# Kernel optimization log

Hardware: AMD Instinct MI355X
Metric: run time of the kernel (lower is better)

## Reference

```python
import jax, jax.numpy as jnp
import numpy as np

B, S, H = 1, 2048, 1024
NH, NKV, HD = 16, 4, 64
I, E, K = 2816, 8, 2
WIN = 512
EPS = 1e-5


def setup_inputs() -> dict:
    key = jax.random.key(0)
    ks = jax.random.split(key, 8)
    sd = 0.02
    return {
        "hidden_states": jax.random.normal(ks[0], (B, S, H), jnp.float32),
        "positions": jnp.arange(S, dtype=jnp.int64),
        "w_qkv": jax.random.normal(ks[1], ((NH + 2 * NKV) * HD, H), jnp.float32) * sd,
        "w_o": jax.random.normal(ks[2], (H, NH * HD), jnp.float32) * sd,
        "router_w": jax.random.normal(ks[3], (E, H), jnp.float32) * sd,
        "ws": jax.random.normal(ks[4], (E, 2 * I, H), jnp.float32) * sd,
        "w2s": jax.random.normal(ks[5], (E, H, I), jnp.float32) * sd,
        "ln1_w": jnp.ones((H,), jnp.float32),
        "ln2_w": jnp.ones((H,), jnp.float32),
    }


def _rmsnorm(x, w):
    return x * jax.lax.rsqrt(jnp.mean(x * x, axis=-1, keepdims=True) + EPS) * w


def reference(hidden_states, positions, w_qkv, w_o, router_w, ws, w2s, ln1_w, ln2_w):
    # residual is None on entry -> residual = input, then input_layernorm
    residual = hidden_states
    x = _rmsnorm(hidden_states, ln1_w)

    # qkv projection (torch Linear: y = x @ W.T), GQA split
    qkv = jnp.einsum("bsh,oh->bso", x, w_qkv)
    q_size, kv_size = NH * HD, NKV * HD
    q = qkv[..., :q_size].reshape(B, S, NH, HD)
    k = qkv[..., q_size:q_size + kv_size].reshape(B, S, NKV, HD)
    v = qkv[..., q_size + kv_size:].reshape(B, S, NKV, HD)
    rep = NH // NKV
    k = jnp.repeat(k, rep, axis=2)  # [B,S,NH,HD]
    v = jnp.repeat(v, rep, axis=2)

    scale = HD ** -0.5
    scores = jnp.einsum("bqhd,bkhd->bhqk", q, k) * scale
    i = jnp.arange(S)[:, None]
    j = jnp.arange(S)[None, :]
    mask = (j <= i) & ((i - j) < WIN)  # causal sliding window
    scores = jnp.where(mask, scores, jnp.finfo(scores.dtype).min)
    attn = jax.nn.softmax(scores, axis=-1)
    o = jnp.einsum("bhqk,bkhd->bqhd", attn, v).reshape(B, S, NH * HD)
    attn_out = jnp.einsum("bso,ho->bsh", o, w_o)

    # pre_moe_layernorm with residual: x += residual; residual = x; x = norm(x)
    x2 = attn_out + residual
    residual2 = x2
    h = _rmsnorm(x2, ln2_w)

    # MoE: router softmax, top-k (renormalize=False), per-expert SwiGLU FFN
    t = h.reshape(-1, H)  # [T,H]
    logits = jnp.einsum("th,eh->te", t, router_w)
    probs = jax.nn.softmax(logits, axis=-1)
    vals, idx = jax.lax.top_k(probs, K)  # [T,K]
    w_dense = jnp.sum(vals[:, :, None] * jax.nn.one_hot(idx, E, dtype=t.dtype), axis=1)  # [T,E]

    out = jnp.zeros_like(t)
    for e in range(E):
        gu = jnp.einsum("th,ih->ti", t, ws[e])  # [T,2I]
        g, u = gu[:, :I], gu[:, I:]
        a = jax.nn.silu(g) * u
        y = jnp.einsum("ti,hi->th", a, w2s[e])
        out = out + w_dense[:, e:e + 1] * y

    return out.reshape(B, S, H), residual2
```

## Files before the change

kernel.cpp:

```cpp
#include <hip/hip_runtime.h>
#include <stdint.h>

typedef unsigned short u16;
typedef __attribute__((ext_vector_type(8))) short short8;
typedef __attribute__((ext_vector_type(4))) float f32x4;

constexpr int SEQ   = 2048;
constexpr int HID   = 1024;
constexpr int NHEAD = 16;
constexpr int QKVD  = 1536;
constexpr int FFI   = 2816;
constexpr int NEXP  = 8;
constexpr int WINSZ = 512;
#define EPSF 1e-5f

__device__ __forceinline__ u16 f2bf(float f) {
  union { unsigned int i; float f; } v; v.f = f;
  unsigned int i = v.i;
  return (u16)((i + 0x7fffu + ((i >> 16) & 1u)) >> 16);
}

__device__ __forceinline__ void gload_lds16(const void* g, void* l) {
  __builtin_amdgcn_global_load_lds((__attribute__((address_space(1))) void*)g,
                                   (__attribute__((address_space(3))) void*)l,
                                   16, 0, 0);
}

#define MFMA_BF16(a, b, c) __builtin_amdgcn_mfma_f32_16x16x32_bf16(a, b, c, 0, 0, 0)

constexpr int CN1 = QKVD * HID / 4;
constexpr int CN2 = HID * HID / 4;
constexpr int CN3 = NEXP * 2 * FFI * HID / 4;
constexpr int CN4 = NEXP * HID * FFI / 4;
constexpr int CN_SMALL = CN1 + CN2;
constexpr int CN_BIG   = CN3 + CN4;
constexpr int NCONV_BLK = CN_BIG / 1024;
constexpr int NATTN_BLK = (SEQ / 64) * NHEAD;

__global__ __launch_bounds__(256) void k_prep(
    const float* __restrict__ x, const float* __restrict__ w, u16* __restrict__ y,
    const float* __restrict__ wqkv, const float* __restrict__ wo,
    u16* __restrict__ dq, u16* __restrict__ dwo) {
  const int bid = blockIdx.x, tid = threadIdx.x;
  __shared__ float red[4];
  if (bid < SEQ) {
    const int wid = tid >> 6, lane = tid & 63;
    const float* xr = x + (size_t)bid * HID;
    float4 v = *(const float4*)&xr[tid * 4];
    float ss = v.x * v.x + v.y * v.y + v.z * v.z + v.w * v.w;
#pragma unroll
    for (int m = 1; m < 64; m <<= 1) ss += __shfl_xor(ss, m);
    if (lane == 0) red[wid] = ss;
    __syncthreads();
    ss = red[0] + red[1] + red[2] + red[3];
    float sc = rsqrtf(ss * (1.0f / HID) + EPSF);
    float4 wv = *(const float4*)&w[tid * 4];
    ushort4 o;
    o.x = f2bf(v.x * sc * wv.x);
    o.y = f2bf(v.y * sc * wv.y);
    o.z = f2bf(v.z * sc * wv.z);
    o.w = f2bf(v.w * sc * wv.w);
    *(ushort4*)&y[(size_t)bid * HID + tid * 4] = o;
    return;
  }
  int j = (bid - SEQ) * 1024 + tid;
#pragma unroll
  for (int t = 0; t < 4; ++t) {
    int i = j + t * 256;
    const float* s; u16* d;
    if (i < CN1) { s = wqkv; d = dq; } else { i -= CN1; s = wo; d = dwo; }
    float4 v = ((const float4*)s)[i];
    ushort4 o;
    o.x = f2bf(v.x); o.y = f2bf(v.y); o.z = f2bf(v.z); o.w = f2bf(v.w);
    ((ushort4*)d)[i] = o;
  }
}

__global__ __launch_bounds__(256, 2) void k_gemm_bt(
    const u16* __restrict__ A, const u16* __restrict__ B,
    void* __restrict__ Cout, int N, int K, int KT, int wf32) {
  __shared__ u16 As[128 * 64];
  __shared__ u16 Bs[64 * 64];
  const int tid = threadIdx.x, wid = tid >> 6, lane = tid & 63;
  const int quad = lane >> 4, l16 = lane & 15;
  const int wr = wid >> 1, wc = wid & 1;
  const int m0 = blockIdx.y * 128, n0 = blockIdx.x * 64;
  const int M = gridDim.y * 128;
  const int kbase = blockIdx.z * KT * 64;
  const int sr = lane >> 3, sc = (lane & 7) * 8;
  f32x4 acc[4][2] = {};
  for (int kt = 0; kt < KT; ++kt) {
    const int k0 = kbase + (kt << 6);
#pragma unroll
    for (int it = 0; it < 4; ++it) {
      int seg = wid * 4 + it;
      int row = seg * 8 + sr;
      gload_lds16(&A[(size_t)(m0 + row) * K + k0 + sc], &As[seg * 512]);
    }
#pragma unroll
    for (int it = 0; it < 2; ++it) {
      int seg = wid * 2 + it;
      int row = seg * 8 + sr;
      gload_lds16(&B[(size_t)(n0 + row) * K + k0 + sc], &Bs[seg * 512]);
    }
    __syncthreads();
#pragma unroll
    for (int ks = 0; ks < 2; ++ks) {
      short8 af[4], bf[2];
#pragma unroll
      for (int t = 0; t < 4; ++t)
        af[t] = *(const short8*)&As[(64 * wr + 16 * t + l16) * 64 + ks * 32 + quad * 8];
#pragma unroll
      for (int t = 0; t < 2; ++t)
        bf[t] = *(const short8*)&Bs[(32 * wc + 16 * t + l16) * 64 + ks * 32 + quad * 8];
#pragma unroll
      for (int mt = 0; mt < 4; ++mt)
#pragma unroll
        for (int nt = 0; nt < 2; ++nt)
          acc[mt][nt] = MFMA_BF16(af[mt], bf[nt], acc[mt][nt]);
    }
    __syncthreads();
  }
  if (wf32) {
    float* C = (float*)Cout + (size_t)blockIdx.z * M * N;
#pragma unroll
    for (int mt = 0; mt < 4; ++mt)
#pragma unroll
      for (int r = 0; r < 4; ++r) {
        int row = m0 + 64 * wr + 16 * mt + quad * 4 + r;
#pragma unroll
        for (int nt = 0; nt < 2; ++nt) {
          int col = n0 + 32 * wc + 16 * nt + l16;
          C[(size_t)row * N + col] = acc[mt][nt][r];
        }
      }
  } else {
    u16* C = (u16*)Cout;
#pragma unroll
    for (int mt = 0; mt < 4; ++mt)
#pragma unroll
      for (int r = 0; r < 4; ++r) {
        int row = m0 + 64 * wr + 16 * mt + quad * 4 + r;
#pragma unroll
        for (int nt = 0; nt < 2; ++nt) {
          int col = n0 + 32 * wc + 16 * nt + l16;
          C[(size_t)row * N + col] = f2bf(acc[mt][nt][r]);
        }
      }
  }
}

__global__ __launch_bounds__(256, 2) void k_attn_conv(
    const u16* __restrict__ qkv, u16* __restrict__ o,
    const float* __restrict__ ws, const float* __restrict__ w2s,
    u16* __restrict__ dws, u16* __restrict__ dw2) {
  const int bid = blockIdx.x;
  const int tid = threadIdx.x;
  if (bid >= NATTN_BLK) {
    int j = (bid - NATTN_BLK) * 1024 + tid;
#pragma unroll
    for (int t = 0; t < 4; ++t) {
      int i = j + t * 256;
      const float* s; u16* d;
      if (i < CN3) { s = ws; d = dws; } else { i -= CN3; s = w2s; d = dw2; }
      float4 v = ((const float4*)s)[i];
      ushort4 u;
      u.x = f2bf(v.x); u.y = f2bf(v.y); u.z = f2bf(v.z); u.w = f2bf(v.w);
      ((ushort4*)d)[i] = u;
    }
    return;
  }
  const int qb = bid & 31;
  const int h  = bid >> 5;
  const int q0 = qb * 64;
  const int g = h >> 2;
  __shared__ u16 Qs[64 * 72], Ks[64 * 72], Vt[64 * 72], Ps[64 * 72];
  const int wid = tid >> 6, lane = tid & 63;
  const int quad = lane >> 4, l16 = lane & 15;

#pragma unroll
  for (int it = 0; it < 2; ++it) {
    int idx = it * 256 + tid;
    int row = idx >> 3, c8 = (idx & 7) * 8;
    *(short8*)&Qs[row * 72 + c8] =
        *(const short8*)&qkv[(size_t)(q0 + row) * QKVD + h * 64 + c8];
  }

  f32x4 oacc[4] = {};
  float mrun[4], lrun[4];
#pragma unroll
  for (int r = 0; r < 4; ++r) { mrun[r] = -1e30f; lrun[r] = 0.f; }

  const int ktlo = (q0 >= WINSZ) ? ((q0 - WINSZ + 1) >> 6) : 0;
  const int kthi = qb;
  for (int kt = ktlo; kt <= kthi; ++kt) {
#pragma unroll
    for (int it = 0; it < 2; ++it) {
      int idx = it * 256 + tid;
      int row = idx >> 3, c8 = (idx & 7) * 8;
      *(short8*)&Ks[row * 72 + c8] =
          *(const short8*)&qkv[(size_t)(kt * 64 + row) * QKVD + 1024 + g * 64 + c8];
    }
#pragma unroll
    for (int it = 0; it < 8; ++it) {
      int idx = it * 256 + tid;
      int key = idx >> 5;
      int d = (idx & 31) * 2;
      unsigned int u = *(const unsigned int*)&qkv[(size_t)(kt * 64 + key) * QKVD + 1280 + g * 64 + d];
      Vt[d * 72 + key] = (u16)(u & 0xffffu);
      Vt[(d + 1) * 72 + key] = (u16)(u >> 16);
    }
    __syncthreads();

    f32x4 sa[4] = {};
#pragma unroll
    for (int ks = 0; ks < 2; ++ks) {
      short8 af = *(const short8*)&Qs[(16 * wid + l16) * 72 + ks * 32 + quad * 8];
#pragma unroll
      for (int ct = 0; ct < 4; ++ct) {
        short8 bf = *(const short8*)&Ks[(16 * ct + l16) * 72 + ks * 32 + quad * 8];
        sa[ct] = MFMA_BF16(af, bf, sa[ct]);
      }
    }

    float pvv[4][4];
#pragma unroll
    for (int r = 0; r < 4; ++r) {
      int i = q0 + 16 * wid + quad * 4 + r;
      float mx = -1e30f;
#pragma unroll
      for (int ct = 0; ct < 4; ++ct) {
        int j = kt * 64 + 16 * ct + l16;
        float v = sa[ct][r] * 0.125f;
        bool ok = (j <= i) && (i - j < WINSZ);
        v = ok ? v : -1e30f;
        pvv[ct][r] = v;
        mx = fmaxf(mx, v);
      }
#pragma unroll
      for (int m = 1; m < 16; m <<= 1) mx = fmaxf(mx, __shfl_xor(mx, m));
      float mnew = fmaxf(mrun[r], mx);
      float alpha = __expf(mrun[r] - mnew);
      float s = 0.f;
#pragma unroll
      for (int ct = 0; ct < 4; ++ct) {
        float p = (pvv[ct][r] > -1e29f) ? __expf(pvv[ct][r] - mnew) : 0.f;
        pvv[ct][r] = p;
        s += p;
      }
#pragma unroll
      for (int m = 1; m < 16; m <<= 1) s += __shfl_xor(s, m);
      lrun[r] = lrun[r] * alpha + s;
      mrun[r] = mnew;
#pragma unroll
      for (int ct = 0; ct < 4; ++ct) oacc[ct][r] *= alpha;
    }
#pragma unroll
    for (int ct = 0; ct < 4; ++ct)
#pragma unroll
      for (int r = 0; r < 4; ++r)
        Ps[(16 * wid + quad * 4 + r) * 72 + 16 * ct + l16] = f2bf(pvv[ct][r]);
    __syncthreads();

#pragma unroll
    for (int ks = 0; ks < 2; ++ks) {
      short8 af = *(const short8*)&Ps[(16 * wid + l16) * 72 + ks * 32 + quad * 8];
#pragma unroll
      for (int ct = 0; ct < 4; ++ct) {
        short8 bf = *(const short8*)&Vt[(16 * ct + l16) * 72 + ks * 32 + quad * 8];
        oacc[ct] = MFMA_BF16(af, bf, oacc[ct]);
      }
    }
    __syncthreads();
  }

#pragma unroll
  for (int ct = 0; ct < 4; ++ct)
#pragma unroll
    for (int r = 0; r < 4; ++r) {
      int row = q0 + 16 * wid + quad * 4 + r;
      float v = oacc[ct][r] / lrun[r];
      o[(size_t)row * HID + h * 64 + 16 * ct + l16] = f2bf(v);
    }
}

__global__ __launch_bounds__(256) void k_rms2_router(
    const float* __restrict__ o0, const float* __restrict__ o1,
    const float* __restrict__ hs, const float* __restrict__ ln2,
    const float* __restrict__ rw, float* __restrict__ out1,
    u16* __restrict__ T, int* __restrict__ counts,
    int* __restrict__ tok_idx, int* __restrict__ tok_slot,
    float* __restrict__ tok_pw) {
  const int tkn = blockIdx.x, tid = threadIdx.x, wid = tid >> 6, lane = tid & 63;
  const size_t base = (size_t)tkn * HID + tid * 4;
  float4 a = *(const float4*)&o0[base];
  float4 b = *(const float4*)&o1[base];
  float4 h = *(const float4*)&hs[base];
  float4 v;
  v.x = a.x + b.x + h.x; v.y = a.y + b.y + h.y;
  v.z = a.z + b.z + h.z; v.w = a.w + b.w + h.w;
  *(float4*)&out1[base] = v;
  float ss = v.x * v.x + v.y * v.y + v.z * v.z + v.w * v.w;
#pragma unroll
  for (int m = 1; m < 64; m <<= 1) ss += __shfl_xor(ss, m);
  __shared__ float red[4];
  if (lane == 0) red[wid] = ss;
  __syncthreads();
  ss = red[0] + red[1] + red[2] + red[3];
  float sc = rsqrtf(ss * (1.0f / HID) + EPSF);
  float4 lw = *(const float4*)&ln2[tid * 4];
  float t0 = v.x * sc * lw.x;
  float t1 = v.y * sc * lw.y;
  float t2 = v.z * sc * lw.z;
  float t3 = v.w * sc * lw.w;
  ushort4 o;
  o.x = f2bf(t0); o.y = f2bf(t1); o.z = f2bf(t2); o.w = f2bf(t3);
  *(ushort4*)&T[(size_t)tkn * HID + tid * 4] = o;

  float p[8];
#pragma unroll
  for (int e = 0; e < 8; ++e) {
    float4 r = *(const float4*)&rw[e * HID + tid * 4];
    p[e] = t0 * r.x + t1 * r.y + t2 * r.z + t3 * r.w;
  }
#pragma unroll
  for (int e = 0; e < 8; ++e)
#pragma unroll
    for (int m = 1; m < 64; m <<= 1) p[e] += __shfl_xor(p[e], m);
  __shared__ float pr[4][8];
  if (lane == 0)
#pragma unroll
    for (int e = 0; e < 8; ++e) pr[wid][e] = p[e];
  __syncthreads();
  if (tid == 0) {
    float lg[8];
#pragma unroll
    for (int e = 0; e < 8; ++e) lg[e] = pr[0][e] + pr[1][e] + pr[2][e] + pr[3][e];
    float mx = lg[0];
#pragma unroll
    for (int e = 1; e < 8; ++e) mx = fmaxf(mx, lg[e]);
    float ex[8], se = 0.f;
#pragma unroll
    for (int e = 0; e < 8; ++e) { ex[e] = __expf(lg[e] - mx); se += ex[e]; }
    int b0 = 0;
#pragma unroll
    for (int e = 1; e < 8; ++e) if (lg[e] > lg[b0]) b0 = e;
    int b1 = (b0 == 0) ? 1 : 0;
#pragma unroll
    for (int e = 0; e < 8; ++e) if (e != b0 && lg[e] > lg[b1]) b1 = e;
    float inv = 1.0f / se;
    int s0 = atomicAdd(&counts[b0], 1);
    tok_idx[b0 * SEQ + s0] = tkn;
    tok_slot[2 * tkn] = b0 * SEQ + s0;
    tok_pw[2 * tkn] = ex[b0] * inv;
    int s1 = atomicAdd(&counts[b1], 1);
    tok_idx[b1 * SEQ + s1] = tkn;
    tok_slot[2 * tkn + 1] = b1 * SEQ + s1;
    tok_pw[2 * tkn + 1] = ex[b1] * inv;
  }
}

__global__ void k_offsets(const int* __restrict__ counts, int* __restrict__ offs) {
  if (threadIdx.x == 0 && blockIdx.x == 0) {
    int s = 0;
    for (int e = 0; e < NEXP; ++e) { offs[e] = s; s += counts[e]; }
    offs[NEXP] = s;
  }
}

__global__ __launch_bounds__(512, 4) void k_moe_gu(
    const u16* __restrict__ T, const u16* __restrict__ Wgu,
    const int* __restrict__ counts, const int* __restrict__ offs,
    const int* __restrict__ tok_idx, u16* __restrict__ Abuf) {
  const int e = blockIdx.z;
  const int cnt = counts[e];
  const int m0 = blockIdx.y * 256;
  if (m0 >= cnt) return;
  const int n0 = blockIdx.x * 64;
  const u16* We = Wgu + (size_t)e * 2 * FFI * HID;
  const int* ti = tok_idx + e * SEQ;
  const int aoff = offs[e];
  __shared__ u16 As[256 * 64], Bg[64 * 64], Bu[64 * 64];
  const int tid = threadIdx.x, wid = tid >> 6, lane = tid & 63;
  const int quad = lane >> 4, l16 = lane & 15;
  const int wr = wid >> 1, wc = wid & 1;
  const int sr = lane >> 3, sc = (lane & 7) * 8;
  int tokrow[4];
#pragma unroll
  for (int it = 0; it < 4; ++it) {
    int row = (wid * 4 + it) * 8 + sr;
    int ra = m0 + row;
    if (ra > cnt - 1) ra = cnt - 1;
    tokrow[it] = ti[ra];
  }
  f32x4 accg[4][2] = {}, accu[4][2] = {};
  for (int kt = 0; kt < 16; ++kt) {
    const int k0 = kt << 6;
#pragma unroll
    for (int it = 0; it < 4; ++it) {
      int seg = wid * 4 + it;
      gload_lds16(&T[(size_t)tokrow[it] * HID + k0 + sc], &As[seg * 512]);
    }
    {
      int row = wid * 8 + sr;
      gload_lds16(&We[(size_t)(n0 + row) * HID + k0 + sc], &Bg[wid * 512]);
      gload_lds16(&We[(size_t)(FFI + n0 + row) * HID + k0 + sc], &Bu[wid * 512]);
    }
    __syncthreads();
#pragma unroll
    for (int ks = 0; ks < 2; ++ks) {
      short8 af[4], bg[2], bu[2];
#pragma unroll
      for (int t = 0; t < 4; ++t)
        af[t] = *(const short8*)&As[(64 * wr + 16 * t + l16) * 64 + ks * 32 + quad * 8];
#pragma unroll
      for (int t = 0; t < 2; ++t) {
        bg[t] = *(const short8*)&Bg[(32 * wc + 16 * t + l16) * 64 + ks * 32 + quad * 8];
        bu[t] = *(const short8*)&Bu[(32 * wc + 16 * t + l16) * 64 + ks * 32 + quad * 8];
      }
#pragma unroll
      for (int mt = 0; mt < 4; ++mt)
#pragma unroll
        for (int nt = 0; nt < 2; ++nt) {
          accg[mt][nt] = MFMA_BF16(af[mt], bg[nt], accg[mt][nt]);
          accu[mt][nt] = MFMA_BF16(af[mt], bu[nt], accu[mt][nt]);
        }
    }
    __syncthreads();
  }
#pragma unroll
  for (int mt = 0; mt < 4; ++mt)
#pragma unroll
    for (int r = 0; r < 4; ++r) {
      int rl = 64 * wr + 16 * mt + quad * 4 + r;
      int grow = m0 + rl;
      if (grow < cnt) {
        size_t rbase = (size_t)(aoff + grow) * FFI;
#pragma unroll
        for (int nt = 0; nt < 2; ++nt) {
          int col = n0 + 32 * wc + 16 * nt + l16;
          float gv = accg[mt][nt][r];
          float uv = accu[mt][nt][r];
          float a = gv / (1.0f + __expf(-gv)) * uv;
          Abuf[rbase + col] = f2bf(a);
        }
      }
    }
}

__global__ __launch_bounds__(256, 2) void k_moe_y(
    const u16* __restrict__ Abuf, const u16* __restrict__ W2,
    const int* __restrict__ counts, const int* __restrict__ offs,
    float* __restrict__ ybuf) {
  const int e = blockIdx.z >> 1;
  const int sk = blockIdx.z & 1;
  const int cnt = counts[e];
  const int m0 = blockIdx.y * 128;
  if (m0 >= cnt) return;
  const int n0 = blockIdx.x * 128;
  const int kbase = sk * 1408;
  const u16* We = W2 + (size_t)e * HID * FFI;
  const int aoff = offs[e];
  __shared__ u16 As[128 * 64], Bs[128 * 64];
  const int tid = threadIdx.x, wid = tid >> 6, lane = tid & 63;
  const int quad = lane >> 4, l16 = lane & 15;
  const int wr = wid >> 1, wc = wid & 1;
  const int sr = lane >> 3, sc = (lane & 7) * 8;
  int arow[4];
#pragma unroll
  for (int it = 0; it < 4; ++it) {
    int row = (wid * 4 + it) * 8 + sr;
    int ra = m0 + row;
    if (ra > cnt - 1) ra = cnt - 1;
    arow[it] = aoff + ra;
  }
  f32x4 acc[4][4] = {};
  for (int kt = 0; kt < 22; ++kt) {
    const int k0 = kbase + (kt << 6);
#pragma unroll
    for (int it = 0; it < 4; ++it) {
      int seg = wid * 4 + it;
      int row = seg * 8 + sr;
      gload_lds16(&Abuf[(size_t)arow[it] * FFI + k0 + sc], &As[seg * 512]);
      gload_lds16(&We[(size_t)(n0 + row) * FFI + k0 + sc], &Bs[seg * 512]);
    }
    __syncthreads();
#pragma unroll
    for (int ks = 0; ks < 2; ++ks) {
      short8 af[4], bf[4];
#pragma unroll
      for (int t = 0; t < 4; ++t)
        af[t] = *(const short8*)&As[(64 * wr + 16 * t + l16) * 64 + ks * 32 + quad * 8];
#pragma unroll
      for (int t = 0; t < 4; ++t)
        bf[t] = *(const short8*)&Bs[(64 * wc + 16 * t + l16) * 64 + ks * 32 + quad * 8];
#pragma unroll
      for (int mt = 0; mt < 4; ++mt)
#pragma unroll
        for (int nt = 0; nt < 4; ++nt)
          acc[mt][nt] = MFMA_BF16(af[mt], bf[nt], acc[mt][nt]);
    }
    __syncthreads();
  }
  float* Y = ybuf + (size_t)sk * 2 * SEQ * HID;
#pragma unroll
  for (int mt = 0; mt < 4; ++mt)
#pragma unroll
    for (int r = 0; r < 4; ++r) {
      int rl = 64 * wr + 16 * mt + quad * 4 + r;
      int grow = m0 + rl;
      if (grow < cnt) {
        size_t obase = (size_t)(aoff + grow) * HID;
#pragma unroll
        for (int nt = 0; nt < 4; ++nt) {
          int col = n0 + 64 * wc + 16 * nt + l16;
          Y[obase + col] = acc[mt][nt][r];
        }
      }
    }
}

__global__ __launch_bounds__(256) void k_moe_out(
    const float* __restrict__ yb, const int* __restrict__ offs,
    const int* __restrict__ tok_slot, const float* __restrict__ tok_pw,
    float* __restrict__ out0) {
  const int t = blockIdx.x, tid = threadIdx.x;
  const int v0 = tok_slot[2 * t], v1 = tok_slot[2 * t + 1];
  const float w0 = tok_pw[2 * t], w1 = tok_pw[2 * t + 1];
  const size_t g0 = (size_t)(offs[v0 >> 11] + (v0 & (SEQ - 1))) * HID;
  const size_t g1 = (size_t)(offs[v1 >> 11] + (v1 & (SEQ - 1))) * HID;
  const size_t YP = (size_t)2 * SEQ * HID;
  const int c = tid * 4;
  float4 a0 = *(const float4*)&yb[g0 + c];
  float4 b0 = *(const float4*)&yb[YP + g0 + c];
  float4 a1 = *(const float4*)&yb[g1 + c];
  float4 b1 = *(const float4*)&yb[YP + g1 + c];
  float4 r;
  r.x = w0 * (a0.x + b0.x) + w1 * (a1.x + b1.x);
  r.y = w0 * (a0.y + b0.y) + w1 * (a1.y + b1.y);
  r.z = w0 * (a0.z + b0.z) + w1 * (a1.z + b1.z);
  r.w = w0 * (a0.w + b0.w) + w1 * (a1.w + b1.w);
  *(float4*)&out0[(size_t)t * HID + c] = r;
}

extern "C" void kernel_launch(void* const* d_in, const int* in_sizes, int n_in,
                              void* d_out, int out_size, void* d_ws, size_t ws_size,
                              hipStream_t stream) {
  const float* hs   = (const float*)d_in[0];
  const float* wqkv = (const float*)d_in[2];
  const float* wo   = (const float*)d_in[3];
  const float* rwt  = (const float*)d_in[4];
  const float* wsx  = (const float*)d_in[5];
  const float* w2s  = (const float*)d_in[6];
  const float* ln1  = (const float*)d_in[7];
  const float* ln2  = (const float*)d_in[8];
  float* out0 = (float*)d_out;
  float* out1 = out0 + (size_t)SEQ * HID;

  char* p = (char*)d_ws;
  u16* xn       = (u16*)p;   p += (size_t)SEQ * HID * 2;
  u16* qkv      = (u16*)p;   p += (size_t)SEQ * QKVD * 2;
  u16* ob       = (u16*)p;   p += (size_t)SEQ * HID * 2;
  float* of     = (float*)p; p += (size_t)2 * SEQ * HID * 4;
  int* counts   = (int*)p;   p += 32;
  int* offs     = (int*)p;   p += 64;
  int* tok_idx  = (int*)p;   p += (size_t)NEXP * SEQ * 4;
  int* tok_slot = (int*)p;   p += (size_t)2 * SEQ * 4;
  float* tok_pw = (float*)p; p += (size_t)2 * SEQ * 4;
  u16* abuf     = (u16*)p;   p += (size_t)2 * SEQ * FFI * 2;
  float* ybuf   = (float*)p; p += (size_t)2 * 2 * SEQ * HID * 4;
  u16* wqkv_b   = (u16*)p;   p += (size_t)QKVD * HID * 2;
  u16* wo_b     = (u16*)p;   p += (size_t)HID * HID * 2;
  u16* ws_b     = (u16*)p;   p += (size_t)NEXP * 2 * FFI * HID * 2;
  u16* w2s_b    = (u16*)p;   p += (size_t)NEXP * HID * FFI * 2;

  u16* tb = xn;

  hipMemsetAsync(counts, 0, 32, stream);

  k_prep<<<SEQ + CN_SMALL / 1024, 256, 0, stream>>>(
      hs, ln1, xn, wqkv, wo, wqkv_b, wo_b);
  k_gemm_bt<<<dim3(QKVD / 64, SEQ / 128, 1), 256, 0, stream>>>(
      xn, wqkv_b, qkv, QKVD, HID, 16, 0);
  k_attn_conv<<<NATTN_BLK + NCONV_BLK, 256, 0, stream>>>(
      qkv, ob, wsx, w2s, ws_b, w2s_b);
  k_gemm_bt<<<dim3(HID / 64, SEQ / 128, 2), 256, 0, stream>>>(
      ob, wo_b, of, HID, HID, 8, 1);
  k_rms2_router<<<SEQ, 256, 0, stream>>>(of, of + (size_t)SEQ * HID, hs, ln2,
                                         rwt, out1, tb, counts, tok_idx,
                                         tok_slot, tok_pw);
  k_offsets<<<1, 64, 0, stream>>>(counts, offs);
  k_moe_gu<<<dim3(FFI / 64, SEQ / 256, NEXP), 512, 0, stream>>>(
      tb, ws_b, counts, offs, tok_idx, abuf);
  k_moe_y<<<dim3(HID / 128, SEQ / 128, NEXP * 2), 256, 0, stream>>>(
      abuf, w2s_b, counts, offs, ybuf);
  k_moe_out<<<SEQ, 256, 0, stream>>>(ybuf, offs, tok_slot, tok_pw, out0);
}
```

Before: 678.6 us.

## Double-buffer LDS tiles in dense and MoE GEMM kernels with vmcnt-based pipelining

Converts the dense GEMM, MoE gate/up, and MoE down-projection kernels from single-buffered LDS loading to a two-stage ping-pong scheme. Each kernel issues the next tile's global-to-LDS loads before computing the current tile, then waits with s_waitcnt vmcnt on only the older loads plus a barrier. This aims to overlap global memory latency with MFMA work. It doubles LDS use per block, and the gate/up kernel's occupancy hint drops from 4 to 2 blocks per CU.

```diff
diff --git a/kernel.cpp b/kernel.cpp
--- a/kernel.cpp
+++ b/kernel.cpp
@@ -27,6 +27,14 @@
 }
 
 #define MFMA_BF16(a, b, c) __builtin_amdgcn_mfma_f32_16x16x32_bf16(a, b, c, 0, 0, 0)
+
+#define PIPE_WAIT(N)                                        \
+  asm volatile("s_waitcnt vmcnt(" #N ")" ::: "memory");     \
+  __builtin_amdgcn_s_barrier();                             \
+  __builtin_amdgcn_sched_barrier(0);
+#define PIPE_END                                            \
+  __builtin_amdgcn_sched_barrier(0);                        \
+  __builtin_amdgcn_s_barrier();
 
 constexpr int CN1 = QKVD * HID / 4;
 constexpr int CN2 = HID * HID / 4;
@@ -79,8 +87,8 @@
 __global__ __launch_bounds__(256, 2) void k_gemm_bt(
     const u16* __restrict__ A, const u16* __restrict__ B,
     void* __restrict__ Cout, int N, int K, int KT, int wf32) {
-  __shared__ u16 As[128 * 64];
-  __shared__ u16 Bs[64 * 64];
+  __shared__ u16 As[2][128 * 64];
+  __shared__ u16 Bs[2][64 * 64];
   const int tid = threadIdx.x, wid = tid >> 6, lane = tid & 63;
   const int quad = lane >> 4, l16 = lane & 15;
   const int wr = wid >> 1, wc = wid & 1;
@@ -89,38 +97,49 @@
   const int kbase = blockIdx.z * KT * 64;
   const int sr = lane >> 3, sc = (lane & 7) * 8;
   f32x4 acc[4][2] = {};
-  for (int kt = 0; kt < KT; ++kt) {
-    const int k0 = kbase + (kt << 6);
-#pragma unroll
-    for (int it = 0; it < 4; ++it) {
-      int seg = wid * 4 + it;
-      int row = seg * 8 + sr;
-      gload_lds16(&A[(size_t)(m0 + row) * K + k0 + sc], &As[seg * 512]);
-    }
-#pragma unroll
-    for (int it = 0; it < 2; ++it) {
-      int seg = wid * 2 + it;
-      int row = seg * 8 + sr;
-      gload_lds16(&B[(size_t)(n0 + row) * K + k0 + sc], &Bs[seg * 512]);
-    }
-    __syncthreads();
-#pragma unroll
-    for (int ks = 0; ks < 2; ++ks) {
-      short8 af[4], bf[2];
-#pragma unroll
-      for (int t = 0; t < 4; ++t)
-        af[t] = *(const short8*)&As[(64 * wr + 16 * t + l16) * 64 + ks * 32 + quad * 8];
-#pragma unroll
-      for (int t = 0; t < 2; ++t)
-        bf[t] = *(const short8*)&Bs[(32 * wc + 16 * t + l16) * 64 + ks * 32 + quad * 8];
-#pragma unroll
-      for (int mt = 0; mt < 4; ++mt)
-#pragma unroll
-        for (int nt = 0; nt < 2; ++nt)
-          acc[mt][nt] = MFMA_BF16(af[mt], bf[nt], acc[mt][nt]);
-    }
-    __syncthreads();
-  }
+
+#define GSTAGE(buf, k0)                                                             \
+  {                                                                                 \
+    _Pragma("unroll") for (int it = 0; it < 4; ++it) {                              \
+      int seg = wid * 4 + it;                                                       \
+      int row = seg * 8 + sr;                                                       \
+      gload_lds16(&A[(size_t)(m0 + row) * K + (k0) + sc], &As[buf][seg * 512]);     \
+    }                                                                               \
+    _Pragma("unroll") for (int it = 0; it < 2; ++it) {                              \
+      int seg = wid * 2 + it;                                                       \
+      int row = seg * 8 + sr;                                                       \
+      gload_lds16(&B[(size_t)(n0 + row) * K + (k0) + sc], &Bs[buf][seg * 512]);     \
+    }                                                                               \
+  }
+#define GCOMP(buf)                                                                  \
+  {                                                                                 \
+    _Pragma("unroll") for (int ks = 0; ks < 2; ++ks) {                              \
+      short8 af[4], bf[2];                                                          \
+      _Pragma("unroll") for (int t = 0; t < 4; ++t)                                 \
+        af[t] = *(const short8*)&As[buf][(64 * wr + 16 * t + l16) * 64 + ks * 32 +  \
+                                         quad * 8];                                 \
+      _Pragma("unroll") for (int t = 0; t < 2; ++t)                                 \
+        bf[t] = *(const short8*)&Bs[buf][(32 * wc + 16 * t + l16) * 64 + ks * 32 +  \
+                                         quad * 8];                                 \
+      _Pragma("unroll") for (int mt = 0; mt < 4; ++mt)                              \
+        _Pragma("unroll") for (int nt = 0; nt < 2; ++nt)                            \
+            acc[mt][nt] = MFMA_BF16(af[mt], bf[nt], acc[mt][nt]);                   \
+    }                                                                               \
+  }
+
+  GSTAGE(0, kbase);
+  int cur = 0;
+  for (int kt = 0; kt < KT - 1; ++kt) {
+    GSTAGE(cur ^ 1, kbase + ((kt + 1) << 6));
+    PIPE_WAIT(6)
+    GCOMP(cur);
+    PIPE_END
+    cur ^= 1;
+  }
+  PIPE_WAIT(0)
+  GCOMP(cur);
+#undef GSTAGE
+#undef GCOMP
   if (wf32) {
     float* C = (float*)Cout + (size_t)blockIdx.z * M * N;
 #pragma unroll
@@ -368,7 +387,7 @@
   }
 }
 
-__global__ __launch_bounds__(512, 4) void k_moe_gu(
+__global__ __launch_bounds__(512, 2) void k_moe_gu(
     const u16* __restrict__ T, const u16* __restrict__ Wgu,
     const int* __restrict__ counts, const int* __restrict__ offs,
     const int* __restrict__ tok_idx, u16* __restrict__ Abuf) {
@@ -380,7 +399,7 @@
   const u16* We = Wgu + (size_t)e * 2 * FFI * HID;
   const int* ti = tok_idx + e * SEQ;
   const int aoff = offs[e];
-  __shared__ u16 As[256 * 64], Bg[64 * 64], Bu[64 * 64];
+  __shared__ u16 As[2][256 * 64], Bg[2][64 * 64], Bu[2][64 * 64];
   const int tid = threadIdx.x, wid = tid >> 6, lane = tid & 63;
   const int quad = lane >> 4, l16 = lane & 15;
   const int wr = wid >> 1, wc = wid & 1;
@@ -394,40 +413,54 @@
     tokrow[it] = ti[ra];
   }
   f32x4 accg[4][2] = {}, accu[4][2] = {};
-  for (int kt = 0; kt < 16; ++kt) {
-    const int k0 = kt << 6;
-#pragma unroll
-    for (int it = 0; it < 4; ++it) {
-      int seg = wid * 4 + it;
-      gload_lds16(&T[(size_t)tokrow[it] * HID + k0 + sc], &As[seg * 512]);
-    }
-    {
-      int row = wid * 8 + sr;
-      gload_lds16(&We[(size_t)(n0 + row) * HID + k0 + sc], &Bg[wid * 512]);
-      gload_lds16(&We[(size_t)(FFI + n0 + row) * HID + k0 + sc], &Bu[wid * 512]);
-    }
-    __syncthreads();
-#pragma unroll
-    for (int ks = 0; ks < 2; ++ks) {
-      short8 af[4], bg[2], bu[2];
-#pragma unroll
-      for (int t = 0; t < 4; ++t)
-        af[t] = *(const short8*)&As[(64 * wr + 16 * t + l16) * 64 + ks * 32 + quad * 8];
-#pragma unroll
-      for (int t = 0; t < 2; ++t) {
-        bg[t] = *(const short8*)&Bg[(32 * wc + 16 * t + l16) * 64 + ks * 32 + quad * 8];
-        bu[t] = *(const short8*)&Bu[(32 * wc + 16 * t + l16) * 64 + ks * 32 + quad * 8];
-      }
-#pragma unroll
-      for (int mt = 0; mt < 4; ++mt)
-#pragma unroll
-        for (int nt = 0; nt < 2; ++nt) {
-          accg[mt][nt] = MFMA_BF16(af[mt], bg[nt], accg[mt][nt]);
-          accu[mt][nt] = MFMA_BF16(af[mt], bu[nt], accu[mt][nt]);
-        }
-    }
-    __syncthreads();
-  }
+
+#define MSTAGE(buf, k0)                                                              \
+  {                                                                                  \
+    _Pragma("unroll") for (int it = 0; it < 4; ++it) {                               \
+      int seg = wid * 4 + it;                                                        \
+      gload_lds16(&T[(size_t)tokrow[it] * HID + (k0) + sc], &As[buf][seg * 512]);    \
+    }                                                                                \
+    {                                                                                \
+      int row = wid * 8 + sr;                                                        \
+      gload_lds16(&We[(size_t)(n0 + row) * HID + (k0) + sc], &Bg[buf][wid * 512]);   \
+      gload_lds16(&We[(size_t)(FFI + n0 + row) * HID + (k0) + sc],                   \
+                  &Bu[buf][wid * 512]);                                              \
+    }                                                                                \
+  }
+#define MCOMP(buf)                                                                   \
+  {                                                                                  \
+    _Pragma("unroll") for (int ks = 0; ks < 2; ++ks) {                               \
+      short8 af[4], bg[2], bu[2];                                                    \
+      _Pragma("unroll") for (int t = 0; t < 4; ++t)                                  \
+        af[t] = *(const short8*)&As[buf][(64 * wr + 16 * t + l16) * 64 + ks * 32 +   \
+                                         quad * 8];                                  \
+      _Pragma("unroll") for (int t = 0; t < 2; ++t) {                                \
+        bg[t] = *(const short8*)&Bg[buf][(32 * wc + 16 * t + l16) * 64 + ks * 32 +   \
+                                         quad * 8];                                  \
+        bu[t] = *(const short8*)&Bu[buf][(32 * wc + 16 * t + l16) * 64 + ks * 32 +   \
+                                         quad * 8];                                  \
+      }                                                                              \
+      _Pragma("unroll") for (int mt = 0; mt < 4; ++mt)                               \
+        _Pragma("unroll") for (int nt = 0; nt < 2; ++nt) {                           \
+          accg[mt][nt] = MFMA_BF16(af[mt], bg[nt], accg[mt][nt]);                    \
+          accu[mt][nt] = MFMA_BF16(af[mt], bu[nt], accu[mt][nt]);                    \
+        }                                                                            \
+    }                                                                                \
+  }
+
+  MSTAGE(0, 0);
+  int cur = 0;
+  for (int kt = 0; kt < 15; ++kt) {
+    MSTAGE(cur ^ 1, (kt + 1) << 6);
+    PIPE_WAIT(6)
+    MCOMP(cur);
+    PIPE_END
+    cur ^= 1;
+  }
+  PIPE_WAIT(0)
+  MCOMP(cur);
+#undef MSTAGE
+#undef MCOMP
 #pragma unroll
   for (int mt = 0; mt < 4; ++mt)
 #pragma unroll
@@ -461,7 +494,7 @@
   const int kbase = sk * 1408;
   const u16* We = W2 + (size_t)e * HID * FFI;
   const int aoff = offs[e];
-  __shared__ u16 As[128 * 64], Bs[128 * 64];
+  __shared__ u16 As[2][128 * 64], Bs[2][128 * 64];
   const int tid = threadIdx.x, wid = tid >> 6, lane = tid & 63;
   const int quad = lane >> 4, l16 = lane & 15;
   const int wr = wid >> 1, wc = wid & 1;
@@ -475,33 +508,45 @@
     arow[it] = aoff + ra;
   }
   f32x4 acc[4][4] = {};
-  for (int kt = 0; kt < 22; ++kt) {
-    const int k0 = kbase + (kt << 6);
-#pragma unroll
-    for (int it = 0; it < 4; ++it) {
-      int seg = wid * 4 + it;
-      int row = seg * 8 + sr;
-      gload_lds16(&Abuf[(size_t)arow[it] * FFI + k0 + sc], &As[seg * 512]);
-      gload_lds16(&We[(size_t)(n0 + row) * FFI + k0 + sc], &Bs[seg * 512]);
-    }
-    __syncthreads();
-#pragma unroll
-    for (int ks = 0; ks < 2; ++ks) {
-      short8 af[4], bf[4];
-#pragma unroll
-      for (int t = 0; t < 4; ++t)
-        af[t] = *(const short8*)&As[(64 * wr + 16 * t + l16) * 64 + ks * 32 + quad * 8];
-#pragma unroll
-      for (int t = 0; t < 4; ++t)
-        bf[t] = *(const short8*)&Bs[(64 * wc + 16 * t + l16) * 64 + ks * 32 + quad * 8];
-#pragma unroll
-      for (int mt = 0; mt < 4; ++mt)
-#pragma unroll
-        for (int nt = 0; nt < 4; ++nt)
-          acc[mt][nt] = MFMA_BF16(af[mt], bf[nt], acc[mt][nt]);
-    }
-    __syncthreads();
-  }
+
+#define YSTAGE(buf, k0)                                                              \
+  {                                                                                  \
+    _Pragma("unroll") for (int it = 0; it < 4; ++it) {                               \
+      int seg = wid * 4 + it;                                                        \
+      int row = seg * 8 + sr;                                                        \
+      gload_lds16(&Abuf[(size_t)arow[it] * FFI + (k0) + sc], &As[buf][seg * 512]);   \
+      gload_lds16(&We[(size_t)(n0 + row) * FFI + (k0) + sc], &Bs[buf][seg * 512]);   \
+    }                                                                                \
+  }
+#define YCOMP(buf)                                                                   \
+  {                                                                                  \
+    _Pragma("unroll") for (int ks = 0; ks < 2; ++ks) {                               \
+      short8 af[4], bf[4];                                                           \
+      _Pragma("unroll") for (int t = 0; t < 4; ++t)                                  \
+        af[t] = *(const short8*)&As[buf][(64 * wr + 16 * t + l16) * 64 + ks * 32 +   \
+                                         quad * 8];                                  \
+      _Pragma("unroll") for (int t = 0; t < 4; ++t)                                  \
+        bf[t] = *(const short8*)&Bs[buf][(64 * wc + 16 * t + l16) * 64 + ks * 32 +   \
+                                         quad * 8];                                  \
+      _Pragma("unroll") for (int mt = 0; mt < 4; ++mt)                               \
+        _Pragma("unroll") for (int nt = 0; nt < 4; ++nt)                             \
+            acc[mt][nt] = MFMA_BF16(af[mt], bf[nt], acc[mt][nt]);                    \
+    }                                                                                \
+  }
+
+  YSTAGE(0, kbase);
+  int cur = 0;
+  for (int kt = 0; kt < 21; ++kt) {
+    YSTAGE(cur ^ 1, kbase + ((kt + 1) << 6));
+    PIPE_WAIT(8)
+    YCOMP(cur);
+    PIPE_END
+    cur ^= 1;
+  }
+  PIPE_WAIT(0)
+  YCOMP(cur);
+#undef YSTAGE
+#undef YCOMP
   float* Y = ybuf + (size_t)sk * 2 * SEQ * HID;
 #pragma unroll
   for (int mt = 0; mt < 4; ++mt)
```

Measured after the change: 659.2 us. -2.9%, faster.

## Fuse fp32-to-bf16 weight conversion into GEMM B-tile loads

Applied to the files above, without the earlier changes.

Drops the standalone passes that convert every weight matrix from fp32 to bf16, including the expert-weight conversion that shared the attention launch. The QKV, O-projection and both MoE GEMMs now read fp32 weights straight from global memory, convert them in registers, and write bf16 into row-padded (stride 72) LDS tiles. This removes the extra write and re-read of the bf16 weight copies and the conversion kernel's blocks. In exchange, each GEMM tile reads twice as many weight bytes per reuse, and the B-tile path loses the asynchronous global-to-LDS loads in favour of synchronous register loads placed before the barrier.

```diff
diff --git a/kernel.cpp b/kernel.cpp
--- a/kernel.cpp
+++ b/kernel.cpp
@@ -20,6 +20,12 @@
   return (u16)((i + 0x7fffu + ((i >> 16) & 1u)) >> 16);
 }
 
+__device__ __forceinline__ ushort4 f2bf4(float4 v) {
+  ushort4 o;
+  o.x = f2bf(v.x); o.y = f2bf(v.y); o.z = f2bf(v.z); o.w = f2bf(v.w);
+  return o;
+}
+
 __device__ __forceinline__ void gload_lds16(const void* g, void* l) {
   __builtin_amdgcn_global_load_lds((__attribute__((address_space(1))) void*)g,
                                    (__attribute__((address_space(3))) void*)l,
@@ -28,59 +34,37 @@
 
 #define MFMA_BF16(a, b, c) __builtin_amdgcn_mfma_f32_16x16x32_bf16(a, b, c, 0, 0, 0)
 
-constexpr int CN1 = QKVD * HID / 4;
-constexpr int CN2 = HID * HID / 4;
-constexpr int CN3 = NEXP * 2 * FFI * HID / 4;
-constexpr int CN4 = NEXP * HID * FFI / 4;
-constexpr int CN_SMALL = CN1 + CN2;
-constexpr int CN_BIG   = CN3 + CN4;
-constexpr int NCONV_BLK = CN_BIG / 1024;
 constexpr int NATTN_BLK = (SEQ / 64) * NHEAD;
 
-__global__ __launch_bounds__(256) void k_prep(
-    const float* __restrict__ x, const float* __restrict__ w, u16* __restrict__ y,
-    const float* __restrict__ wqkv, const float* __restrict__ wo,
-    u16* __restrict__ dq, u16* __restrict__ dwo) {
+__global__ __launch_bounds__(256) void k_prep(const float* __restrict__ x,
+                                              const float* __restrict__ w,
+                                              u16* __restrict__ y) {
   const int bid = blockIdx.x, tid = threadIdx.x;
+  const int wid = tid >> 6, lane = tid & 63;
   __shared__ float red[4];
-  if (bid < SEQ) {
-    const int wid = tid >> 6, lane = tid & 63;
-    const float* xr = x + (size_t)bid * HID;
-    float4 v = *(const float4*)&xr[tid * 4];
-    float ss = v.x * v.x + v.y * v.y + v.z * v.z + v.w * v.w;
-#pragma unroll
-    for (int m = 1; m < 64; m <<= 1) ss += __shfl_xor(ss, m);
-    if (lane == 0) red[wid] = ss;
-    __syncthreads();
-    ss = red[0] + red[1] + red[2] + red[3];
-    float sc = rsqrtf(ss * (1.0f / HID) + EPSF);
-    float4 wv = *(const float4*)&w[tid * 4];
-    ushort4 o;
-    o.x = f2bf(v.x * sc * wv.x);
-    o.y = f2bf(v.y * sc * wv.y);
-    o.z = f2bf(v.z * sc * wv.z);
-    o.w = f2bf(v.w * sc * wv.w);
-    *(ushort4*)&y[(size_t)bid * HID + tid * 4] = o;
-    return;
-  }
-  int j = (bid - SEQ) * 1024 + tid;
-#pragma unroll
-  for (int t = 0; t < 4; ++t) {
-    int i = j + t * 256;
-    const float* s; u16* d;
-    if (i < CN1) { s = wqkv; d = dq; } else { i -= CN1; s = wo; d = dwo; }
-    float4 v = ((const float4*)s)[i];
-    ushort4 o;
-    o.x = f2bf(v.x); o.y = f2bf(v.y); o.z = f2bf(v.z); o.w = f2bf(v.w);
-    ((ushort4*)d)[i] = o;
-  }
+  const float* xr = x + (size_t)bid * HID;
+  float4 v = *(const float4*)&xr[tid * 4];
+  float ss = v.x * v.x + v.y * v.y + v.z * v.z + v.w * v.w;
+#pragma unroll
+  for (int m = 1; m < 64; m <<= 1) ss += __shfl_xor(ss, m);
+  if (lane == 0) red[wid] = ss;
+  __syncthreads();
+  ss = red[0] + red[1] + red[2] + red[3];
+  float sc = rsqrtf(ss * (1.0f / HID) + EPSF);
+  float4 wv = *(const float4*)&w[tid * 4];
+  ushort4 o;
+  o.x = f2bf(v.x * sc * wv.x);
+  o.y = f2bf(v.y * sc * wv.y);
+  o.z = f2bf(v.z * sc * wv.z);
+  o.w = f2bf(v.w * sc * wv.w);
+  *(ushort4*)&y[(size_t)bid * HID + tid * 4] = o;
 }
 
 __global__ __launch_bounds__(256, 2) void k_gemm_bt(
-    const u16* __restrict__ A, const u16* __restrict__ B,
+    const u16* __restrict__ A, const float* __restrict__ B,
     void* __restrict__ Cout, int N, int K, int KT, int wf32) {
   __shared__ u16 As[128 * 64];
-  __shared__ u16 Bs[64 * 64];
+  __shared__ u16 Bs[64 * 72];
   const int tid = threadIdx.x, wid = tid >> 6, lane = tid & 63;
   const int quad = lane >> 4, l16 = lane & 15;
   const int wr = wid >> 1, wc = wid & 1;
@@ -88,21 +72,26 @@
   const int M = gridDim.y * 128;
   const int kbase = blockIdx.z * KT * 64;
   const int sr = lane >> 3, sc = (lane & 7) * 8;
+  const int brow = wid * 16 + (lane >> 2);
+  const int bk = (lane & 3) * 16;
   f32x4 acc[4][2] = {};
   for (int kt = 0; kt < KT; ++kt) {
     const int k0 = kbase + (kt << 6);
+    const float* bp = &B[(size_t)(n0 + brow) * K + k0 + bk];
+    float4 bv0 = *(const float4*)&bp[0];
+    float4 bv1 = *(const float4*)&bp[4];
+    float4 bv2 = *(const float4*)&bp[8];
+    float4 bv3 = *(const float4*)&bp[12];
 #pragma unroll
     for (int it = 0; it < 4; ++it) {
       int seg = wid * 4 + it;
       int row = seg * 8 + sr;
       gload_lds16(&A[(size_t)(m0 + row) * K + k0 + sc], &As[seg * 512]);
     }
-#pragma unroll
-    for (int it = 0; it < 2; ++it) {
-      int seg = wid * 2 + it;
-      int row = seg * 8 + sr;
-      gload_lds16(&B[(size_t)(n0 + row) * K + k0 + sc], &Bs[seg * 512]);
-    }
+    *(ushort4*)&Bs[brow * 72 + bk + 0]  = f2bf4(bv0);
+    *(ushort4*)&Bs[brow * 72 + bk + 4]  = f2bf4(bv1);
+    *(ushort4*)&Bs[brow * 72 + bk + 8]  = f2bf4(bv2);
+    *(ushort4*)&Bs[brow * 72 + bk + 12] = f2bf4(bv3);
     __syncthreads();
 #pragma unroll
     for (int ks = 0; ks < 2; ++ks) {
@@ -112,7 +101,7 @@
         af[t] = *(const short8*)&As[(64 * wr + 16 * t + l16) * 64 + ks * 32 + quad * 8];
 #pragma unroll
       for (int t = 0; t < 2; ++t)
-        bf[t] = *(const short8*)&Bs[(32 * wc + 16 * t + l16) * 64 + ks * 32 + quad * 8];
+        bf[t] = *(const short8*)&Bs[(32 * wc + 16 * t + l16) * 72 + ks * 32 + quad * 8];
 #pragma unroll
       for (int mt = 0; mt < 4; ++mt)
 #pragma unroll
@@ -150,26 +139,10 @@
   }
 }
 
-__global__ __launch_bounds__(256, 2) void k_attn_conv(
-    const u16* __restrict__ qkv, u16* __restrict__ o,
-    const float* __restrict__ ws, const float* __restrict__ w2s,
-    u16* __restrict__ dws, u16* __restrict__ dw2) {
+__global__ __launch_bounds__(256, 2) void k_attn(const u16* __restrict__ qkv,
+                                                 u16* __restrict__ o) {
   const int bid = blockIdx.x;
   const int tid = threadIdx.x;
-  if (bid >= NATTN_BLK) {
-    int j = (bid - NATTN_BLK) * 1024 + tid;
-#pragma unroll
-    for (int t = 0; t < 4; ++t) {
-      int i = j + t * 256;
-      const float* s; u16* d;
-      if (i < CN3) { s = ws; d = dws; } else { i -= CN3; s = w2s; d = dw2; }
-      float4 v = ((const float4*)s)[i];
-      ushort4 u;
-      u.x = f2bf(v.x); u.y = f2bf(v.y); u.z = f2bf(v.z); u.w = f2bf(v.w);
-      ((ushort4*)d)[i] = u;
-    }
-    return;
-  }
   const int qb = bid & 31;
   const int h  = bid >> 5;
   const int q0 = qb * 64;
@@ -369,7 +342,7 @@
 }
 
 __global__ __launch_bounds__(512, 4) void k_moe_gu(
-    const u16* __restrict__ T, const u16* __restrict__ Wgu,
+    const u16* __restrict__ T, const float* __restrict__ Wgu,
     const int* __restrict__ counts, const int* __restrict__ offs,
     const int* __restrict__ tok_idx, u16* __restrict__ Abuf) {
   const int e = blockIdx.z;
@@ -377,14 +350,16 @@
   const int m0 = blockIdx.y * 256;
   if (m0 >= cnt) return;
   const int n0 = blockIdx.x * 64;
-  const u16* We = Wgu + (size_t)e * 2 * FFI * HID;
+  const float* We = Wgu + (size_t)e * 2 * FFI * HID;
   const int* ti = tok_idx + e * SEQ;
   const int aoff = offs[e];
-  __shared__ u16 As[256 * 64], Bg[64 * 64], Bu[64 * 64];
+  __shared__ u16 As[256 * 64], Bg[64 * 72], Bu[64 * 72];
   const int tid = threadIdx.x, wid = tid >> 6, lane = tid & 63;
   const int quad = lane >> 4, l16 = lane & 15;
   const int wr = wid >> 1, wc = wid & 1;
   const int sr = lane >> 3, sc = (lane & 7) * 8;
+  const int brow = wid * 8 + (lane >> 3);
+  const int bk = (lane & 7) * 8;
   int tokrow[4];
 #pragma unroll
   for (int it = 0; it < 4; ++it) {
@@ -396,16 +371,21 @@
   f32x4 accg[4][2] = {}, accu[4][2] = {};
   for (int kt = 0; kt < 16; ++kt) {
     const int k0 = kt << 6;
+    const float* gp = &We[(size_t)(n0 + brow) * HID + k0 + bk];
+    const float* up = &We[(size_t)(FFI + n0 + brow) * HID + k0 + bk];
+    float4 g0 = *(const float4*)&gp[0];
+    float4 g1 = *(const float4*)&gp[4];
+    float4 u0 = *(const float4*)&up[0];
+    float4 u1 = *(const float4*)&up[4];
 #pragma unroll
     for (int it = 0; it < 4; ++it) {
       int seg = wid * 4 + it;
       gload_lds16(&T[(size_t)tokrow[it] * HID + k0 + sc], &As[seg * 512]);
     }
-    {
-      int row = wid * 8 + sr;
-      gload_lds16(&We[(size_t)(n0 + row) * HID + k0 + sc], &Bg[wid * 512]);
-      gload_lds16(&We[(size_t)(FFI + n0 + row) * HID + k0 + sc], &Bu[wid * 512]);
-    }
+    *(ushort4*)&Bg[brow * 72 + bk + 0] = f2bf4(g0);
+    *(ushort4*)&Bg[brow * 72 + bk + 4] = f2bf4(g1);
+    *(ushort4*)&Bu[brow * 72 + bk + 0] = f2bf4(u0);
+    *(ushort4*)&Bu[brow * 72 + bk + 4] = f2bf4(u1);
     __syncthreads();
 #pragma unroll
     for (int ks = 0; ks < 2; ++ks) {
@@ -415,8 +395,8 @@
         af[t] = *(const short8*)&As[(64 * wr + 16 * t + l16) * 64 + ks * 32 + quad * 8];
 #pragma unroll
       for (int t = 0; t < 2; ++t) {
-        bg[t] = *(const short8*)&Bg[(32 * wc + 16 * t + l16) * 64 + ks * 32 + quad * 8];
-        bu[t] = *(const short8*)&Bu[(32 * wc + 16 * t + l16) * 64 + ks * 32 + quad * 8];
+        bg[t] = *(const short8*)&Bg[(32 * wc + 16 * t + l16) * 72 + ks * 32 + quad * 8];
+        bu[t] = *(const short8*)&Bu[(32 * wc + 16 * t + l16) * 72 + ks * 32 + quad * 8];
       }
 #pragma unroll
       for (int mt = 0; mt < 4; ++mt)
@@ -449,7 +429,7 @@
 }
 
 __global__ __launch_bounds__(256, 2) void k_moe_y(
-    const u16* __restrict__ Abuf, const u16* __restrict__ W2,
+    const u16* __restrict__ Abuf, const float* __restrict__ W2,
     const int* __restrict__ counts, const int* __restrict__ offs,
     float* __restrict__ ybuf) {
   const int e = blockIdx.z >> 1;
@@ -459,13 +439,15 @@
   if (m0 >= cnt) return;
   const int n0 = blockIdx.x * 128;
   const int kbase = sk * 1408;
-  const u16* We = W2 + (size_t)e * HID * FFI;
+  const float* We = W2 + (size_t)e * HID * FFI;
   const int aoff = offs[e];
-  __shared__ u16 As[128 * 64], Bs[128 * 64];
+  __shared__ u16 As[128 * 64], Bs[128 * 72];
   const int tid = threadIdx.x, wid = tid >> 6, lane = tid & 63;
   const int quad = lane >> 4, l16 = lane & 15;
   const int wr = wid >> 1, wc = wid & 1;
   const int sr = lane >> 3, sc = (lane & 7) * 8;
+  const int brow = wid * 32 + (lane >> 1);
+  const int bk = (lane & 1) * 32;
   int arow[4];
 #pragma unroll
   for (int it = 0; it < 4; ++it) {
@@ -477,13 +459,18 @@
   f32x4 acc[4][4] = {};
   for (int kt = 0; kt < 22; ++kt) {
     const int k0 = kbase + (kt << 6);
+    const float* bp = &We[(size_t)(n0 + brow) * FFI + k0 + bk];
+    float4 bv[8];
+#pragma unroll
+    for (int j = 0; j < 8; ++j) bv[j] = *(const float4*)&bp[4 * j];
 #pragma unroll
     for (int it = 0; it < 4; ++it) {
       int seg = wid * 4 + it;
-      int row = seg * 8 + sr;
       gload_lds16(&Abuf[(size_t)arow[it] * FFI + k0 + sc], &As[seg * 512]);
-      gload_lds16(&We[(size_t)(n0 + row) * FFI + k0 + sc], &Bs[seg * 512]);
-    }
+    }
+#pragma unroll
+    for (int j = 0; j < 8; ++j)
+      *(ushort4*)&Bs[brow * 72 + bk + 4 * j] = f2bf4(bv[j]);
     __syncthreads();
 #pragma unroll
     for (int ks = 0; ks < 2; ++ks) {
@@ -493,7 +480,7 @@
         af[t] = *(const short8*)&As[(64 * wr + 16 * t + l16) * 64 + ks * 32 + quad * 8];
 #pragma unroll
       for (int t = 0; t < 4; ++t)
-        bf[t] = *(const short8*)&Bs[(64 * wc + 16 * t + l16) * 64 + ks * 32 + quad * 8];
+        bf[t] = *(const short8*)&Bs[(64 * wc + 16 * t + l16) * 72 + ks * 32 + quad * 8];
 #pragma unroll
       for (int mt = 0; mt < 4; ++mt)
 #pragma unroll
@@ -569,30 +556,24 @@
   float* tok_pw = (float*)p; p += (size_t)2 * SEQ * 4;
   u16* abuf     = (u16*)p;   p += (size_t)2 * SEQ * FFI * 2;
   float* ybuf   = (float*)p; p += (size_t)2 * 2 * SEQ * HID * 4;
-  u16* wqkv_b   = (u16*)p;   p += (size_t)QKVD * HID * 2;
-  u16* wo_b     = (u16*)p;   p += (size_t)HID * HID * 2;
-  u16* ws_b     = (u16*)p;   p += (size_t)NEXP * 2 * FFI * HID * 2;
-  u16* w2s_b    = (u16*)p;   p += (size_t)NEXP * HID * FFI * 2;
 
   u16* tb = xn;
 
   hipMemsetAsync(counts, 0, 32, stream);
 
-  k_prep<<<SEQ + CN_SMALL / 1024, 256, 0, stream>>>(
-      hs, ln1, xn, wqkv, wo, wqkv_b, wo_b);
+  k_prep<<<SEQ, 256, 0, stream>>>(hs, ln1, xn);
   k_gemm_bt<<<dim3(QKVD / 64, SEQ / 128, 1), 256, 0, stream>>>(
-      xn, wqkv_b, qkv, QKVD, HID, 16, 0);
-  k_attn_conv<<<NATTN_BLK + NCONV_BLK, 256, 0, stream>>>(
-      qkv, ob, wsx, w2s, ws_b, w2s_b);
+      xn, wqkv, qkv, QKVD, HID, 16, 0);
+  k_attn<<<NATTN_BLK, 256, 0, stream>>>(qkv, ob);
   k_gemm_bt<<<dim3(HID / 64, SEQ / 128, 2), 256, 0, stream>>>(
-      ob, wo_b, of, HID, HID, 8, 1);
+      ob, wo, of, HID, HID, 8, 1);
   k_rms2_router<<<SEQ, 256, 0, stream>>>(of, of + (size_t)SEQ * HID, hs, ln2,
                                          rwt, out1, tb, counts, tok_idx,
                                          tok_slot, tok_pw);
   k_offsets<<<1, 64, 0, stream>>>(counts, offs);
   k_moe_gu<<<dim3(FFI / 64, SEQ / 256, NEXP), 512, 0, stream>>>(
-      tb, ws_b, counts, offs, tok_idx, abuf);
+      tb, wsx, counts, offs, tok_idx, abuf);
   k_moe_y<<<dim3(HID / 128, SEQ / 128, NEXP * 2), 256, 0, stream>>>(
-      abuf, w2s_b, counts, offs, ybuf);
+      abuf, w2s, counts, offs, ybuf);
   k_moe_out<<<SEQ, 256, 0, stream>>>(ybuf, offs, tok_slot, tok_pw, out0);
 }
```

After: 687.3 us. About the same (+1.3%).
